# Performance work log

Hardware: AMD Instinct MI355X
Metric: run time of the kernel (lower is better)

The kernel has to match this reference:

```python
import jax, jax.numpy as jnp
import numpy as np
from jax import lax

IN_DIM = 256
MID = IN_DIM // 2          # 128
NUM_FILTERS = 8
OUT_DIM = 256
EMBED_DIM = 256
BN_EPS = 1e-5


def star_relu(x, scale, bias):
    # StarReLU: s * relu(x)**2 + b
    return scale * jnp.square(jax.nn.relu(x)) + bias


def setup_inputs() -> dict:
    key = jax.random.key(0)
    ks = jax.random.split(key, 12)
    B, H, W = 2, 16, 16
    h, w = 128, 128
    inp = {
        "x": jax.random.normal(ks[0], (B, IN_DIM, H, W), jnp.float32),
        "y": jax.random.normal(ks[1], (B, OUT_DIM, h, w), jnp.float32),
        # feature_fuse: 1x1 conv, depthwise 3x3 conv, BatchNorm (eval-mode stats)
        "conv1_w": jax.random.normal(ks[2], (MID, IN_DIM), jnp.float32) * 0.02,
        "conv1_b": jnp.zeros((MID,), jnp.float32),
        "dw_w": jax.random.normal(ks[3], (MID, 3, 3), jnp.float32) * 0.02,
        "dw_b": jnp.zeros((MID,), jnp.float32),
        "bn_gamma": jnp.ones((MID,), jnp.float32),
        "bn_beta": jnp.zeros((MID,), jnp.float32),
        "bn_mean": jax.random.normal(ks[4], (MID,), jnp.float32) * 0.1,
        "bn_var": jax.random.uniform(ks[5], (MID,), jnp.float32, 0.5, 1.5),
        "sr1_scale": jnp.ones((1,), jnp.float32),
        "sr1_bias": jnp.zeros((1,), jnp.float32),
        # channle_expand 1x1 conv
        "ce_w": jax.random.normal(ks[6], (NUM_FILTERS, MID), jnp.float32) * 0.02,
        "ce_b": jnp.zeros((NUM_FILTERS,), jnp.float32),
        "sr2_scale": jnp.ones((1,), jnp.float32),
        "sr2_bias": jnp.zeros((1,), jnp.float32),
        "W_base": jax.random.normal(ks[7], (OUT_DIM * EMBED_DIM, NUM_FILTERS), jnp.float32) * 0.02,
    }
    return inp


def reference(x, y, conv1_w, conv1_b, dw_w, dw_b, bn_gamma, bn_beta, bn_mean,
              bn_var, sr1_scale, sr1_bias, ce_w, ce_b, sr2_scale, sr2_bias, W_base):
    B, _, fh, fw = x.shape
    b, c, h, w = y.shape
    ph, pw = h // fh, w // fw

    # feature_fuse
    t = jnp.einsum('bchw,oc->bohw', x, conv1_w) + conv1_b[None, :, None, None]
    t = lax.conv_general_dilated(
        t, dw_w[:, None, :, :], (1, 1), ((1, 1), (1, 1)),
        feature_group_count=MID,
        dimension_numbers=('NCHW', 'OIHW', 'NCHW')) + dw_b[None, :, None, None]
    t = bn_gamma[None, :, None, None] * (t - bn_mean[None, :, None, None]) \
        * lax.rsqrt(bn_var + BN_EPS)[None, :, None, None] + bn_beta[None, :, None, None]
    t = star_relu(t, sr1_scale, sr1_bias)

    # channle_expand + act -> per-location filter coefficients [b, F, fh, fw]
    wdec = star_relu(jnp.einsum('bchw,fc->bfhw', t, ce_w) + ce_b[None, :, None, None],
                     sr2_scale, sr2_bias)

    # hypernetwork: [b, E*O, fh, fw], flattened as (embed_dim, out_dim)
    Wd = jnp.einsum('bfhw,ef->behw', wdec, W_base)
    Wd = Wd.reshape(b, EMBED_DIM, OUT_DIM, fh, fw)

    # massive-group 1x1 conv == per-(batch, block) small GEMM over spatial patches
    yb = y.reshape(b, c, fh, ph, fw, pw)
    out = jnp.einsum('beoij,boipjq->beipjq', Wd, yb)  # [b, E, fh, ph, fw, pw]
    return out.reshape(b, EMBED_DIM, h, w)
```

## Files before the change

kernel.cpp:

```cpp
#include <hip/hip_runtime.h>
#include <stdint.h>

typedef unsigned short u16t;
typedef unsigned int   u32t;
typedef _Float16       h16;
typedef __attribute__((ext_vector_type(2))) _Float16 h16x2;
typedef __attribute__((ext_vector_type(8))) short    short8;
typedef __attribute__((ext_vector_type(4))) float    f32x4;

#if defined(__has_builtin)
#if __has_builtin(__builtin_amdgcn_fdot2)
#define HAVE_DOT2 1
#endif
#endif

__device__ __forceinline__ float dot2h(u32t a, u32t b, float c){
#ifdef HAVE_DOT2
  return __builtin_amdgcn_fdot2(__builtin_bit_cast(h16x2, a),
                                __builtin_bit_cast(h16x2, b), c, false);
#else
  h16x2 ha = __builtin_bit_cast(h16x2, a), hb = __builtin_bit_cast(h16x2, b);
  return c + (float)ha[0]*(float)hb[0] + (float)ha[1]*(float)hb[1];
#endif
}

__device__ __forceinline__ float bf2f(u16t h){
  union { u32t u; float f; } c; c.u = ((u32t)h) << 16; return c.f;
}
__device__ __forceinline__ u32t pk2bf(float a, float b){
  u32t ua = __builtin_bit_cast(u32t, a) + 0x8000u;
  u32t ub = __builtin_bit_cast(u32t, b) + 0x8000u;
  return __builtin_amdgcn_perm(ub, ua, 0x07060302u);
}
__device__ __forceinline__ u32t pk2h(float a, float b){
  h16x2 h = { (h16)a, (h16)b };
  return __builtin_bit_cast(u32t, h);
}

template<bool BF>
__device__ __forceinline__ float ldv(const void* p, size_t i){
  if constexpr (BF) return bf2f(((const u16t*)p)[i]);
  else              return ((const float*)p)[i];
}
template<bool BF>
__device__ __forceinline__ void ld8(const void* p, size_t i, float* v){
  if constexpr (BF){
    uint4 u = *(const uint4*)((const u16t*)p + i);
    const u32t a[4] = {u.x, u.y, u.z, u.w};
#pragma unroll
    for (int d = 0; d < 4; ++d){
      v[2*d]   = bf2f((u16t)(a[d] & 0xffffu));
      v[2*d+1] = bf2f((u16t)(a[d] >> 16));
    }
  } else {
    const float4* q = (const float4*)((const float*)p + i);
    float4 A = q[0], B = q[1];
    v[0]=A.x; v[1]=A.y; v[2]=A.z; v[3]=A.w;
    v[4]=B.x; v[5]=B.y; v[6]=B.z; v[7]=B.w;
  }
}

__device__ __forceinline__ bool probe_bf(const void* xv){
  const u16t* p = (const u16t*)xv;
  const int lane = threadIdx.x & 63;
  const u16t h0 = p[lane], h1 = p[lane + 64];
  const int e0 = (h0 >> 7) & 0xff, e1 = (h1 >> 7) & 0xff;
  unsigned long long b0 = __ballot(e0 >= 90 && e0 <= 150);
  unsigned long long b1 = __ballot(e1 >= 90 && e1 <= 150);
  return (__popcll(b0) + __popcll(b1)) >= 104;
}

template<bool BF>
__device__ __forceinline__ void pre12_body(
    const void* x, const void* w, const void* bias,
    const void* dww, const void* dwb,
    const void* bng, const void* bnb, const void* bnm, const void* bnv,
    const void* s1s, const void* s1b, float* t2, float (*ts)[256], int bq)
{
  const int b = bq >> 5, cq = bq & 31;
  const int cl = threadIdx.x >> 8, ij = threadIdx.x & 255;
  const int c = cq * 4 + cl;
  const int i = ij >> 4, j = ij & 15;
  float a0 = ldv<BF>(bias, c);
  const size_t xb = (size_t)b * 65536 + ij;
#pragma unroll 8
  for (int k = 0; k < 256; ++k)
    a0 += ldv<BF>(x, xb + (size_t)k * 256) * ldv<BF>(w, (size_t)c * 256 + k);
  ts[cl][ij] = a0;
  __syncthreads();
  float s = ldv<BF>(dwb, c);
#pragma unroll
  for (int di = 0; di < 3; ++di){
    const int ii = i + di - 1;
    if (ii < 0 || ii > 15) continue;
#pragma unroll
    for (int dj = 0; dj < 3; ++dj){
      const int jj = j + dj - 1;
      if (jj < 0 || jj > 15) continue;
      s += ts[cl][ii * 16 + jj] * ldv<BF>(dww, c * 9 + di * 3 + dj);
    }
  }
  const float v = ldv<BF>(bng, c) * (s - ldv<BF>(bnm, c)) *
                  rsqrtf(ldv<BF>(bnv, c) + 1e-5f) + ldv<BF>(bnb, c);
  const float r = fmaxf(v, 0.0f);
  t2[((size_t)b * 128 + c) * 256 + ij] = ldv<BF>(s1s, 0) * r * r + ldv<BF>(s1b, 0);
}

template<bool BF>
__device__ __forceinline__ void prew_body(const void* wb, uint4* wbh2, int pb){
  const int t = pb * 1024 + threadIdx.x;
  const int e = t & 255, o = t >> 8;
  float v[8];
  ld8<BF>(wb, ((size_t)e * 256 + o) * 8, v);
  wbh2[(size_t)o * 256 + e] = make_uint4(pk2h(v[0], v[1]), pk2h(v[2], v[3]),
                                         pk2h(v[4], v[5]), pk2h(v[6], v[7]));
}

__global__ __launch_bounds__(1024) void k_fused(
    const void* x,
    const void* w1, const void* b1, const void* dww, const void* dwb,
    const void* bng, const void* bnb, const void* bnm, const void* bnv,
    const void* s1s, const void* s1b, const void* wb,
    float* t2, uint4* wbh2)
{
  __shared__ float ts[4][256];
  const bool bf = probe_bf(x);
  const int bid = blockIdx.x;
  if (bid < 64){
    if (bf) pre12_body<true >(x,w1,b1,dww,dwb,bng,bnb,bnm,bnv,s1s,s1b,t2,ts,bid);
    else    pre12_body<false>(x,w1,b1,dww,dwb,bng,bnb,bnm,bnv,s1s,s1b,t2,ts,bid);
  } else {
    if (bf) prew_body<true >(wb, wbh2, bid - 64);
    else    prew_body<false>(wb, wbh2, bid - 64);
  }
}

template<bool BF>
__device__ __forceinline__ void main_body(
    const void* y, const float* t2, const void* cew, const void* ceb,
    const void* s2s, const void* s2b,
    const uint4* wbh2, float* out, u16t* smem)
{
  const int bid = blockIdx.x;
  const int b = bid >> 7, i = (bid >> 3) & 15, jp = bid & 7, j0 = jp * 2;
  const int tid = threadIdx.x;
  const int wv = tid >> 6, lane = tid & 63;

  const int w4 = tid & 3, p = (tid >> 2) & 7, opq = tid >> 5;

  float fA[2][4], fB[2][4];
  u32t  uA[2][2], uB[2][2];

  auto issue_loads = [&](int cs, int buf){
    const int o = (cs * 32 + opq) * 2;
    const size_t base = (((size_t)(b * 256 + o) * 128) + i * 8 + p) * 128
                      + jp * 16 + w4 * 4;
    if constexpr (BF){
      const u16t* yp = (const u16t*)y;
      const uint2 u0 = *(const uint2*)(yp + base);
      const uint2 u1 = *(const uint2*)(yp + base + 16384);
      uA[buf][0] = u0.x; uA[buf][1] = u0.y;
      uB[buf][0] = u1.x; uB[buf][1] = u1.y;
    } else {
      const float* yp = (const float*)y;
      const float4 A = *(const float4*)(yp + base);
      const float4 B = *(const float4*)(yp + base + 16384);
      fA[buf][0]=A.x; fA[buf][1]=A.y; fA[buf][2]=A.z; fA[buf][3]=A.w;
      fB[buf][0]=B.x; fB[buf][1]=B.y; fB[buf][2]=B.z; fB[buf][3]=B.w;
    }
  };
  auto write_chunk = [&](int cs, int buf){
    u32t pk[4];
    if constexpr (BF){
#pragma unroll
      for (int d = 0; d < 2; ++d){
        const u32t lo = uA[buf][d], hi = uB[buf][d];
        pk[2*d]   = (lo & 0xffffu) | (hi << 16);
        pk[2*d+1] = (lo >> 16)     | (hi & 0xffff0000u);
      }
    } else {
#pragma unroll
      for (int k = 0; k < 4; ++k) pk[k] = pk2bf(fA[buf][k], fB[buf][k]);
    }
    const int o  = (cs * 32 + opq) * 2;
    const int oc = o >> 3, osub = o & 7;
#pragma unroll
    for (int k = 0; k < 4; ++k){
      const int w_l  = w4 * 4 + k;
      const int row  = (w_l >> 3) * 64 + p * 8 + (w_l & 7);
      const int phys = (oc + row) & 31;
      *(u32t*)(smem + row * 256 + phys * 8 + osub) = pk[k];
    }
  };

  issue_loads(0, 0);
  issue_loads(1, 1);

  float* wds = (float*)(smem + 32768);

  if (tid < 64){
    const int g = (tid >> 5) & 1, f = (tid >> 2) & 7, cq = tid & 3;
    const int ij = i * 16 + j0 + g;
    const float* tp = t2 + (size_t)b * 32768 + ij;
    float a = 0.0f;
#pragma unroll 8
    for (int c = cq; c < 128; c += 4)
      a += tp[(size_t)c * 256] * ldv<BF>(cew, (size_t)f * 128 + c);
    a += __shfl_xor(a, 1);
    a += __shfl_xor(a, 2);
    if (cq == 0){
      const float tot = a + ldv<BF>(ceb, f);
      const float rr  = fmaxf(tot, 0.0f);
      wds[g * 8 + f] = ldv<BF>(s2s, 0) * rr * rr + ldv<BF>(s2b, 0);
    }
  }

  write_chunk(0, 0);

  const int l15 = lane & 15, l4 = lane >> 4;
  const int e0  = wv * 16;

  const uint4* wrow = wbh2 + (size_t)(l4 * 8) * 256 + e0 + l15;

  f32x4 acc[2][4];
#pragma unroll
  for (int g = 0; g < 2; ++g)
#pragma unroll
    for (int nt = 0; nt < 4; ++nt)
      acc[g][nt] = (f32x4){0.f, 0.f, 0.f, 0.f};

  u32t wdp[2][4];

#pragma unroll
  for (int cs = 0; cs < 4; ++cs){
    __syncthreads();
    if (cs == 0){
#pragma unroll
      for (int g = 0; g < 2; ++g)
#pragma unroll
        for (int d = 0; d < 4; ++d)
          wdp[g][d] = pk2h(wds[g * 8 + 2 * d], wds[g * 8 + 2 * d + 1]);
    }
    if (cs + 2 <= 3) issue_loads(cs + 2, cs & 1);
    if (cs + 1 <= 3) write_chunk(cs + 1, (cs + 1) & 1);

#pragma unroll
    for (int kh = 0; kh < 2; ++kh){
      const int ks = cs * 2 + kh;
      uint4 Wb[8];
#pragma unroll
      for (int r = 0; r < 8; ++r) Wb[r] = wrow[(size_t)(ks * 32 + r) * 256];
      float s[2][8];
#pragma unroll
      for (int r = 0; r < 8; ++r){
        const uint4 w4r = Wb[r];
#pragma unroll
        for (int g = 0; g < 2; ++g){
          float t = dot2h(w4r.x, wdp[g][0], 0.0f);
          t = dot2h(w4r.y, wdp[g][1], t);
          t = dot2h(w4r.z, wdp[g][2], t);
          s[g][r] = dot2h(w4r.w, wdp[g][3], t);
        }
      }
#pragma unroll
      for (int g = 0; g < 2; ++g){
        u32t a4[4];
#pragma unroll
        for (int d = 0; d < 4; ++d) a4[d] = pk2bf(s[g][2*d], s[g][2*d+1]);
        const short8 af = __builtin_bit_cast(short8, *(uint4*)a4);
#pragma unroll
        for (int nt = 0; nt < 4; ++nt){
          const int row  = g * 64 + nt * 16 + l15;
          const int phys = (ks * 4 + l4 + row) & 31;
          const short8 bfr = *(const short8*)(smem + row * 256 + phys * 8);
          acc[g][nt] = __builtin_amdgcn_mfma_f32_16x16x32_bf16(af, bfr, acc[g][nt], 0, 0, 0);
        }
      }
    }
  }

#pragma unroll
  for (int g = 0; g < 2; ++g){
#pragma unroll
    for (int nt = 0; nt < 4; ++nt){
      const int col = nt * 16 + l15;
      const int pp = col >> 3, qq = col & 7;
#pragma unroll
      for (int r = 0; r < 4; ++r){
        const int ee = e0 + l4 * 4 + r;
        const size_t oaddr = ((size_t)(b * 256 + ee) * 128 + (i * 8 + pp)) * 128
                           + (j0 + g) * 8 + qq;
        out[oaddr] = acc[g][nt][r];
      }
    }
  }
}
__global__ __launch_bounds__(1024, 4) void k_main(
    const void* x, const void* y, const float* t2, const void* cew, const void* ceb,
    const void* s2s, const void* s2b,
    const uint4* wbh2, float* out)
{
  extern __shared__ __align__(16) u16t smem[];
  if (probe_bf(x)) main_body<true >(y, t2, cew, ceb, s2s, s2b, wbh2, out, smem);
  else             main_body<false>(y, t2, cew, ceb, s2s, s2b, wbh2, out, smem);
}

extern "C" void kernel_launch(void* const* d_in, const int* in_sizes, int n_in,
                              void* d_out, int out_size, void* d_ws, size_t ws_size,
                              hipStream_t stream)
{
  float* t2    = (float*)d_ws;
  uint4* wbh2  = (uint4*)((char*)d_ws + 262144);

  k_fused<<<dim3(128), dim3(1024), 0, stream>>>(
      d_in[0], d_in[2], d_in[3], d_in[4], d_in[5], d_in[6], d_in[7],
      d_in[8], d_in[9], d_in[10], d_in[11], d_in[16], t2, wbh2);

  const int lds_bytes = 65536 + 64;
  hipFuncSetAttribute((const void*)k_main,
                      hipFuncAttributeMaxDynamicSharedMemorySize, lds_bytes);
  k_main<<<dim3(256), dim3(1024), lds_bytes, stream>>>(
      d_in[0], d_in[1], t2, d_in[12], d_in[13], d_in[14], d_in[15],
      wbh2, (float*)d_out);
}
```

Before: 154.6 us.

## Split embed dimension across two 512-thread blocks and simplify y staging pipeline

The main kernel now launches 512 blocks of 512 threads instead of 256 blocks of 1024 threads. Each pair of blocks covers the same spatial tile and takes one half of the embed dimension. Each block still stages the full y tile into LDS, so global y reads are duplicated within a pair. Adjacent pair indices are meant to make the second read hit cache. The y prefetch changes from two chunks in flight to one chunk loaded during compute and written to LDS after the MFMA loop. The goal is finer-grained scheduling and possibly two resident blocks per CU, at the cost of redundant y traffic and redundant wdec computation.

```diff
diff --git a/kernel.cpp b/kernel.cpp
--- a/kernel.cpp
+++ b/kernel.cpp
@@ -142,59 +142,68 @@
     const uint4* wbh2, float* out, u16t* smem)
 {
   const int bid = blockIdx.x;
-  const int b = bid >> 7, i = (bid >> 3) & 15, jp = bid & 7, j0 = jp * 2;
+  const int ec  = (bid >> 3) & 1;
+  const int gx  = (bid & 7) | ((bid >> 4) << 3);
+  const int b = gx >> 7, i = (gx >> 3) & 15, jp = gx & 7, j0 = jp * 2;
   const int tid = threadIdx.x;
   const int wv = tid >> 6, lane = tid & 63;
 
-  const int w4 = tid & 3, p = (tid >> 2) & 7, opq = tid >> 5;
+  const int w4 = tid & 3, p = (tid >> 2) & 7, oph = tid >> 5;
 
   float fA[2][4], fB[2][4];
   u32t  uA[2][2], uB[2][2];
 
-  auto issue_loads = [&](int cs, int buf){
-    const int o = (cs * 32 + opq) * 2;
-    const size_t base = (((size_t)(b * 256 + o) * 128) + i * 8 + p) * 128
-                      + jp * 16 + w4 * 4;
-    if constexpr (BF){
-      const u16t* yp = (const u16t*)y;
-      const uint2 u0 = *(const uint2*)(yp + base);
-      const uint2 u1 = *(const uint2*)(yp + base + 16384);
-      uA[buf][0] = u0.x; uA[buf][1] = u0.y;
-      uB[buf][0] = u1.x; uB[buf][1] = u1.y;
-    } else {
-      const float* yp = (const float*)y;
-      const float4 A = *(const float4*)(yp + base);
-      const float4 B = *(const float4*)(yp + base + 16384);
-      fA[buf][0]=A.x; fA[buf][1]=A.y; fA[buf][2]=A.z; fA[buf][3]=A.w;
-      fB[buf][0]=B.x; fB[buf][1]=B.y; fB[buf][2]=B.z; fB[buf][3]=B.w;
+  auto issue_loads = [&](int cs){
+#pragma unroll
+    for (int s = 0; s < 2; ++s){
+      const int opq = oph + s * 16;
+      const int o = (cs * 32 + opq) * 2;
+      const size_t base = (((size_t)(b * 256 + o) * 128) + i * 8 + p) * 128
+                        + jp * 16 + w4 * 4;
+      if constexpr (BF){
+        const u16t* yp = (const u16t*)y;
+        const uint2 u0 = *(const uint2*)(yp + base);
+        const uint2 u1 = *(const uint2*)(yp + base + 16384);
+        uA[s][0] = u0.x; uA[s][1] = u0.y;
+        uB[s][0] = u1.x; uB[s][1] = u1.y;
+      } else {
+        const float* yp = (const float*)y;
+        const float4 A = *(const float4*)(yp + base);
+        const float4 B = *(const float4*)(yp + base + 16384);
+        fA[s][0]=A.x; fA[s][1]=A.y; fA[s][2]=A.z; fA[s][3]=A.w;
+        fB[s][0]=B.x; fB[s][1]=B.y; fB[s][2]=B.z; fB[s][3]=B.w;
+      }
     }
   };
-  auto write_chunk = [&](int cs, int buf){
-    u32t pk[4];
-    if constexpr (BF){
-#pragma unroll
-      for (int d = 0; d < 2; ++d){
-        const u32t lo = uA[buf][d], hi = uB[buf][d];
-        pk[2*d]   = (lo & 0xffffu) | (hi << 16);
-        pk[2*d+1] = (lo >> 16)     | (hi & 0xffff0000u);
-      }
-    } else {
-#pragma unroll
-      for (int k = 0; k < 4; ++k) pk[k] = pk2bf(fA[buf][k], fB[buf][k]);
-    }
-    const int o  = (cs * 32 + opq) * 2;
-    const int oc = o >> 3, osub = o & 7;
-#pragma unroll
-    for (int k = 0; k < 4; ++k){
-      const int w_l  = w4 * 4 + k;
-      const int row  = (w_l >> 3) * 64 + p * 8 + (w_l & 7);
-      const int phys = (oc + row) & 31;
-      *(u32t*)(smem + row * 256 + phys * 8 + osub) = pk[k];
+  auto write_chunk = [&](int cs){
+#pragma unroll
+    for (int s = 0; s < 2; ++s){
+      u32t pk[4];
+      if constexpr (BF){
+#pragma unroll
+        for (int d = 0; d < 2; ++d){
+          const u32t lo = uA[s][d], hi = uB[s][d];
+          pk[2*d]   = (lo & 0xffffu) | (hi << 16);
+          pk[2*d+1] = (lo >> 16)     | (hi & 0xffff0000u);
+        }
+      } else {
+#pragma unroll
+        for (int k = 0; k < 4; ++k) pk[k] = pk2bf(fA[s][k], fB[s][k]);
+      }
+      const int opq = oph + s * 16;
+      const int o  = (cs * 32 + opq) * 2;
+      const int oc = o >> 3, osub = o & 7;
+#pragma unroll
+      for (int k = 0; k < 4; ++k){
+        const int w_l  = w4 * 4 + k;
+        const int row  = (w_l >> 3) * 64 + p * 8 + (w_l & 7);
+        const int phys = (oc + row) & 31;
+        *(u32t*)(smem + row * 256 + phys * 8 + osub) = pk[k];
+      }
     }
   };
 
-  issue_loads(0, 0);
-  issue_loads(1, 1);
+  issue_loads(0);
 
   float* wds = (float*)(smem + 32768);
 
@@ -215,10 +224,10 @@
     }
   }
 
-  write_chunk(0, 0);
+  write_chunk(0);
 
   const int l15 = lane & 15, l4 = lane >> 4;
-  const int e0  = wv * 16;
+  const int e0  = ec * 128 + wv * 16;
 
   const uint4* wrow = wbh2 + (size_t)(l4 * 8) * 256 + e0 + l15;
 
@@ -241,8 +250,7 @@
         for (int d = 0; d < 4; ++d)
           wdp[g][d] = pk2h(wds[g * 8 + 2 * d], wds[g * 8 + 2 * d + 1]);
     }
-    if (cs + 2 <= 3) issue_loads(cs + 2, cs & 1);
-    if (cs + 1 <= 3) write_chunk(cs + 1, (cs + 1) & 1);
+    if (cs < 3) issue_loads(cs + 1);
 
 #pragma unroll
     for (int kh = 0; kh < 2; ++kh){
@@ -277,6 +285,7 @@
         }
       }
     }
+    if (cs < 3) write_chunk(cs + 1);
   }
 
 #pragma unroll
@@ -295,7 +304,7 @@
     }
   }
 }
-__global__ __launch_bounds__(1024, 4) void k_main(
+__global__ __launch_bounds__(512, 4) void k_main(
     const void* x, const void* y, const float* t2, const void* cew, const void* ceb,
     const void* s2s, const void* s2b,
     const uint4* wbh2, float* out)
@@ -319,7 +328,7 @@
   const int lds_bytes = 65536 + 64;
   hipFuncSetAttribute((const void*)k_main,
                       hipFuncAttributeMaxDynamicSharedMemorySize, lds_bytes);
-  k_main<<<dim3(256), dim3(1024), lds_bytes, stream>>>(
+  k_main<<<dim3(512), dim3(512), lds_bytes, stream>>>(
       d_in[0], d_in[1], t2, d_in[12], d_in[13], d_in[14], d_in[15],
       wbh2, (float*)d_out);
 }
```

After: 153.5 us. About the same (-0.7%).
